# Kernel tuning notes

Measured on AMD Instinct MI355X. Metric: run time of the kernel, lower is better.

## Reference

```python
import jax, jax.numpy as jnp
import numpy as np

EPS = 1e-5


def _gcn_conv(x, src, dst, norm, W, b, n_nodes):
    # PyG GCNConv: transform, then normalized scatter-add aggregation (self-loops included in src/dst)
    h = x @ W                                   # [N, out]
    msg = h[src] * norm[:, None]                # gather over edges [E+N, out]
    agg = jax.ops.segment_sum(msg, dst, num_segments=n_nodes)
    return agg + b


def _bn(x, gamma, beta):
    # BatchNorm1d in training mode: batch stats over node axis, biased variance
    mu = jnp.mean(x, axis=0)
    var = jnp.mean((x - mu) ** 2, axis=0)
    return (x - mu) * jax.lax.rsqrt(var + EPS) * gamma + beta


def setup_inputs() -> dict:
    key = jax.random.key(0)
    ks = jax.random.split(key, 8)
    N, E, F_in, H, F_out = 50000, 800000, 32, 96, 2
    x = jax.random.normal(ks[0], (N, F_in), dtype=jnp.float32)
    edge_index = jax.random.randint(ks[1], (2, E), 0, N, dtype=jnp.int64)
    def lin(k, fi, fo):
        s = 1.0 / np.sqrt(fi)
        return jax.random.uniform(k, (fi, fo), jnp.float32, -s, s)
    W1 = lin(ks[2], F_in, H); b1 = jnp.zeros((H,), jnp.float32)
    W2 = lin(ks[3], H, H);    b2 = jnp.zeros((H,), jnp.float32)
    W3 = lin(ks[4], H, H);    b3 = jnp.zeros((H,), jnp.float32)
    W4 = lin(ks[5], H, F_out); b4 = jnp.zeros((F_out,), jnp.float32)
    g1 = jnp.ones((H,), jnp.float32); be1 = jnp.zeros((H,), jnp.float32)
    g2 = jnp.ones((H,), jnp.float32); be2 = jnp.zeros((H,), jnp.float32)
    g3 = jnp.ones((H,), jnp.float32); be3 = jnp.zeros((H,), jnp.float32)
    return dict(x=x, edge_index=edge_index,
                W1=W1, b1=b1, g1=g1, be1=be1,
                W2=W2, b2=b2, g2=g2, be2=be2,
                W3=W3, b3=b3, g3=g3, be3=be3,
                W4=W4, b4=b4)


def reference(x, edge_index, W1, b1, g1, be1, W2, b2, g2, be2, W3, b3, g3, be3, W4, b4):
    N = x.shape[0]
    loop = jnp.arange(N, dtype=edge_index.dtype)
    src = jnp.concatenate([edge_index[0], loop])   # add self-loops
    dst = jnp.concatenate([edge_index[1], loop])
    deg = jax.ops.segment_sum(jnp.ones_like(dst, dtype=x.dtype), dst, num_segments=N)
    dinv = jnp.where(deg > 0, jax.lax.rsqrt(deg), 0.0)
    norm = dinv[src] * dinv[dst]                   # D^{-1/2} (A+I) D^{-1/2}

    h = jax.nn.relu(_bn(_gcn_conv(x, src, dst, norm, W1, b1, N), g1, be1))
    h = jax.nn.relu(_bn(_gcn_conv(h, src, dst, norm, W2, b2, N), g2, be2))
    h = jax.nn.relu(_bn(_gcn_conv(h, src, dst, norm, W3, b3, N), g3, be3))
    return _gcn_conv(h, src, dst, norm, W4, b4, N)
```

## Files before the change

### kernel.cpp

```cpp
#include <hip/hip_runtime.h>
#include <hip/hip_bf16.h>

using bf16x8 = __attribute__((ext_vector_type(8))) short;
using f32x4  = __attribute__((ext_vector_type(4))) float;

__device__ __forceinline__ float ldf(const void* p, size_t i, float isf){
  if (isf > 0.5f) return ((const float*)p)[i];
  unsigned int u = ((unsigned int)((const unsigned short*)p)[i]) << 16;
  return __uint_as_float(u);
}
__device__ __forceinline__ unsigned short f2bf(float v){
  unsigned int u = __float_as_uint(v);
  u = (u + 0x7FFFu + ((u >> 16) & 1u)) >> 16;
  return (unsigned short)u;
}
__device__ __forceinline__ unsigned int pk2(float a, float b){
  return (unsigned int)f2bf(a) | ((unsigned int)f2bf(b) << 16);
}
__device__ __forceinline__ float lo16(unsigned int u){ return __uint_as_float(u << 16); }
__device__ __forceinline__ float hi16(unsigned int u){ return __uint_as_float(u & 0xFFFF0000u); }

__global__ void k_fill(unsigned short* o, unsigned short v, int n){
  int i = blockIdx.x*blockDim.x + threadIdx.x;
  if (i < n) o[i] = v;
}

__global__ void k_prep(const unsigned short* xh, const unsigned int* eu,
                       float* flag, int nelemX, long long E,
                       const void* W1, const void* W2, const void* W3, const void* W4,
                       unsigned short* __restrict__ Wt1, unsigned short* __restrict__ Wt2,
                       unsigned short* __restrict__ Wt3, float* __restrict__ W4f,
                       int* __restrict__ cnt, float* __restrict__ stAll, int n){
  int t = threadIdx.x;
  if (blockIdx.x > 0){
    int total = n + 4608;
    for (int i = (int)(blockIdx.x-1)*256 + t; i < total; i += (int)(gridDim.x-1)*256){
      if (i < n) cnt[i] = 0; else stAll[i - n] = 0.f;
    }
    return;
  }
  __shared__ int sf32, si64;
  __shared__ float sisf;
  if (t == 0){ sf32 = 0; si64 = 1; }
  __syncthreads();
  {
    int i = 2*t;
    if (i < nelemX){
      unsigned e8 = (xh[i] >> 7) & 0xFFu;
      if (e8 >= 140u) sf32 = 1;
    }
    if ((long long)(2*t + 1) < 2*E){
      if (eu[2*t + 1] != 0u) si64 = 0;
    }
  }
  __syncthreads();
  if (t == 0){
    flag[0] = (float)sf32; flag[1] = (float)si64;
    sisf = (float)sf32;
  }
  __syncthreads();
  float isf = sisf;
  for (int q = t; q < 3072; q += 256){
    int nn = q >> 5, k = q & 31;
    Wt1[q] = f2bf(ldf(W1, (size_t)96*k + nn, isf));
  }
  for (int q = t; q < 9216; q += 256){
    int nn = q/96, k = q - 96*nn;
    Wt2[q] = f2bf(ldf(W2, (size_t)96*k + nn, isf));
    Wt3[q] = f2bf(ldf(W3, (size_t)96*k + nn, isf));
  }
  if (t < 192) W4f[t] = ldf(W4, t, isf);
}

__global__ void k_cnt(const int* __restrict__ ei, const float* __restrict__ flag,
                      int* __restrict__ cnt, long long E, int n){
  long long i = (long long)blockIdx.x*blockDim.x + threadIdx.x;
  if (i >= E) return;
  int d = (flag[1] > 0.5f) ? ei[2*E + 2*i] : ei[E + i];
  if ((unsigned)d < (unsigned)n) atomicAdd(&cnt[d], 1);
}

__global__ void k_scan(const int* __restrict__ cnt, int* __restrict__ rowst,
                       int* __restrict__ cursor, float* __restrict__ dinv, int n){
  __shared__ int woff[16];
  __shared__ int chtot;
  __shared__ int carry_s;
  int tid = threadIdx.x;
  int lane = tid & 63, wid = tid >> 6;
  if (tid == 0) carry_s = 0;
  __syncthreads();
  for (int base = 0; base < n; base += 1024){
    int i = base + tid;
    int v = (i < n) ? cnt[i] : 0;
    int s = v;
    #pragma unroll
    for (int off = 1; off < 64; off <<= 1){
      int u = __shfl_up(s, off, 64);
      if (lane >= off) s += u;
    }
    if (lane == 63) woff[wid] = s;
    __syncthreads();
    if (tid < 16){
      int w = woff[tid];
      int ws_ = w;
      #pragma unroll
      for (int off = 1; off < 16; off <<= 1){
        int u = __shfl_up(ws_, off, 64);
        if (tid >= off) ws_ += u;
      }
      woff[tid] = ws_ - w;
      if (tid == 15) chtot = ws_;
    }
    __syncthreads();
    int carry = carry_s;
    if (i < n){
      int r = carry + woff[wid] + s - v;
      rowst[i] = r;
      cursor[i] = r;
      dinv[i]  = rsqrtf((float)(1 + v));
    }
    __syncthreads();
    if (tid == 0) carry_s = carry + chtot;
  }
  __syncthreads();
  if (tid == 0) rowst[n] = carry_s;
}

#define FS_CHUNK 4096
template<typename IT>
__global__ __launch_bounds__(256) void k_fl1(const int* __restrict__ ei,
      const float* __restrict__ flag, int* __restrict__ cursor, IT* __restrict__ csr,
      long long E, int n, int gF8,
      const void* __restrict__ x, const unsigned short* __restrict__ Wt1b,
      const float* __restrict__ dinv, unsigned short* __restrict__ HS){
  __shared__ __align__(16) unsigned short Xs[64][40];
  __shared__ __align__(16) unsigned short Wt[96][40];
  int t = threadIdx.x;
  if ((int)blockIdx.x < gF8){
    int part = blockIdx.x & 7;
    long long base = (long long)(blockIdx.x >> 3) * FS_CHUNK;
    int pl = (int)(((long long)n *  part     ) >> 3);
    int pr = (int)(((long long)n * (part + 1)) >> 3);
    bool i64 = (flag[1] > 0.5f);
    long long lim = base + FS_CHUNK < E ? base + FS_CHUNK : E;
    for (long long i = base + t; i < lim; i += 256){
      int s, d;
      if (i64){ s = ei[2*i]; d = ei[2*E + 2*i]; }
      else    { s = ei[i];   d = ei[E + i];     }
      if (d >= pl && d < pr && (unsigned)s < (unsigned)n){
        int p = atomicAdd(&cursor[d], 1);
        csr[p] = (IT)s;
      }
    }
    return;
  }
  int bid = blockIdx.x - gF8;
  float isf = flag[0];
  for (int q = t; q < 384; q += 256){
    uint4 v = ((const uint4*)Wt1b)[q];
    *(uint4*)&Wt[q >> 2][(q & 3)*8] = v;
  }
  {
    int row = t >> 2, part = t & 3;
    int node = bid*64 + row;
    uint4 o;
    if (node < n){
      if (isf > 0.5f){
        const float* xr = (const float*)x + (size_t)32*node + 8*part;
        o.x = pk2(xr[0], xr[1]); o.y = pk2(xr[2], xr[3]);
        o.z = pk2(xr[4], xr[5]); o.w = pk2(xr[6], xr[7]);
      } else {
        o = ((const uint4*)x)[(size_t)4*node + part];
      }
    } else { o.x = o.y = o.z = o.w = 0u; }
    *(uint4*)&Xs[row][8*part] = o;
  }
  __syncthreads();

  int wv = t >> 6, lane = t & 63;
  int m = lane & 15, quad = lane >> 4;
  bf16x8 av = *(const bf16x8*)&Xs[16*wv + m][8*quad];
  f32x4 acc[6];
  #pragma unroll
  for (int c = 0; c < 6; ++c) acc[c] = (f32x4)(0.f);
  #pragma unroll
  for (int c = 0; c < 6; ++c){
    bf16x8 bv = *(const bf16x8*)&Wt[16*c + m][8*quad];
    acc[c] = __builtin_amdgcn_mfma_f32_16x16x32_bf16(av, bv, acc[c], 0, 0, 0);
  }
  int rowbase = bid*64 + 16*wv + 4*quad;
  float div[4];
  #pragma unroll
  for (int r = 0; r < 4; ++r){ int rr = rowbase + r; div[r] = (rr < n) ? dinv[rr] : 0.f; }
  #pragma unroll
  for (int c = 0; c < 6; ++c){
    int col = 16*c + m;
    #pragma unroll
    for (int r = 0; r < 4; ++r){
      int rr = rowbase + r;
      if (rr < n) HS[(size_t)96*rr + col] = f2bf(acc[c][r]*div[r]);
    }
  }
}

#define ACC8(v) { a0+=lo16((v).x); a1+=hi16((v).x); a2+=lo16((v).y); a3+=hi16((v).y); \
                  a4+=lo16((v).z); a5+=hi16((v).z); a6+=lo16((v).w); a7+=hi16((v).w); }
template<typename IT>
__global__ __launch_bounds__(192) void k_agg(const uint4* __restrict__ hsr,
      const int* __restrict__ rowst, const IT* __restrict__ csr,
      const float* __restrict__ dinv, uint4* __restrict__ zb4,
      float* __restrict__ stout, int n){
  __shared__ float ls[16][97], lq[16][97];
  int g = threadIdx.x, ty = threadIdx.y;
  int t = ty*12 + g;
  int node = blockIdx.x*16 + ty;
  float r[8];
  if (node < n){
    uint4 v = hsr[(size_t)node*12 + g];
    float a0 = lo16(v.x), a1 = hi16(v.x), a2 = lo16(v.y), a3 = hi16(v.y);
    float a4 = lo16(v.z), a5 = hi16(v.z), a6 = lo16(v.w), a7 = hi16(v.w);
    int b = rowst[node], e = rowst[node+1];
    int j = b;
    for (; j + 7 < e; j += 8){
      uint4 v0 = hsr[(size_t)csr[j]  *12 + g];
      uint4 v1 = hsr[(size_t)csr[j+1]*12 + g];
      uint4 v2 = hsr[(size_t)csr[j+2]*12 + g];
      uint4 v3 = hsr[(size_t)csr[j+3]*12 + g];
      uint4 v4 = hsr[(size_t)csr[j+4]*12 + g];
      uint4 v5 = hsr[(size_t)csr[j+5]*12 + g];
      uint4 v6 = hsr[(size_t)csr[j+6]*12 + g];
      uint4 v7 = hsr[(size_t)csr[j+7]*12 + g];
      ACC8(v0); ACC8(v1); ACC8(v2); ACC8(v3);
      ACC8(v4); ACC8(v5); ACC8(v6); ACC8(v7);
    }
    for (; j + 3 < e; j += 4){
      uint4 v0 = hsr[(size_t)csr[j]  *12 + g];
      uint4 v1 = hsr[(size_t)csr[j+1]*12 + g];
      uint4 v2 = hsr[(size_t)csr[j+2]*12 + g];
      uint4 v3 = hsr[(size_t)csr[j+3]*12 + g];
      ACC8(v0); ACC8(v1); ACC8(v2); ACC8(v3);
    }
    for (; j < e; ++j){
      uint4 vv = hsr[(size_t)csr[j]*12 + g];
      ACC8(vv);
    }
    float di = dinv[node];
    uint4 o;
    o.x = pk2(a0*di, a1*di);
    o.y = pk2(a2*di, a3*di);
    o.z = pk2(a4*di, a5*di);
    o.w = pk2(a6*di, a7*di);
    zb4[(size_t)node*12 + g] = o;
    r[0]=lo16(o.x); r[1]=hi16(o.x); r[2]=lo16(o.y); r[3]=hi16(o.y);
    r[4]=lo16(o.z); r[5]=hi16(o.z); r[6]=lo16(o.w); r[7]=hi16(o.w);
  } else {
    #pragma unroll
    for (int jj = 0; jj < 8; ++jj) r[jj] = 0.f;
  }
  #pragma unroll
  for (int jj = 0; jj < 8; ++jj){
    ls[ty][8*g + jj] = r[jj];
    lq[ty][8*g + jj] = r[jj]*r[jj];
  }
  __syncthreads();
  if (t < 96){
    float s = 0.f, q = 0.f;
    #pragma unroll
    for (int rr = 0; rr < 16; ++rr){ s += ls[rr][t]; q += lq[rr][t]; }
    int rep = blockIdx.x & 7;
    atomicAdd(&stout[192*rep + t],      s);
    atomicAdd(&stout[192*rep + 96 + t], q);
  }
}

__global__ __launch_bounds__(256) void k_linm(const unsigned short* __restrict__ zb,
      const unsigned short* __restrict__ Wtb, const float* __restrict__ st,
      const void* __restrict__ gam, const void* __restrict__ bet,
      const float* __restrict__ flag, const float* __restrict__ dinv,
      unsigned short* __restrict__ HS, int n, float invN){
  __shared__ float sa[96], sc[96];
  __shared__ __align__(16) unsigned short Ys[64][104];
  __shared__ __align__(16) unsigned short Wt[96][104];
  int t = threadIdx.x;
  if (t < 96){
    float ssum = 0.f, qsum = 0.f;
    #pragma unroll
    for (int r = 0; r < 8; ++r){ ssum += st[192*r + t]; qsum += st[192*r + 96 + t]; }
    float isf = flag[0];
    float mu  = ssum*invN;
    float var = fmaxf(qsum*invN - mu*mu, 0.f);
    float istd = rsqrtf(var + 1e-5f);
    float a = ldf(gam, t, isf)*istd;
    sa[t] = a; sc[t] = ldf(bet, t, isf) - mu*a;
  }
  for (int q = t; q < 1152; q += 256){
    uint4 v = ((const uint4*)Wtb)[q];
    *(uint4*)&Wt[q/12][8*(q - 12*(q/12))] = v;
  }
  __syncthreads();
  {
    int row = t >> 2, part = t & 3;
    int node = blockIdx.x*64 + row;
    if (node < n){
      const uint4* zr = (const uint4*)(zb + (size_t)96*node) + 3*part;
      #pragma unroll
      for (int q = 0; q < 3; ++q){
        uint4 zz = zr[q];
        int k = 24*part + 8*q;
        float y0 = fmaxf(lo16(zz.x)*sa[k]   + sc[k],   0.f);
        float y1 = fmaxf(hi16(zz.x)*sa[k+1] + sc[k+1], 0.f);
        float y2 = fmaxf(lo16(zz.y)*sa[k+2] + sc[k+2], 0.f);
        float y3 = fmaxf(hi16(zz.y)*sa[k+3] + sc[k+3], 0.f);
        float y4 = fmaxf(lo16(zz.z)*sa[k+4] + sc[k+4], 0.f);
        float y5 = fmaxf(hi16(zz.z)*sa[k+5] + sc[k+5], 0.f);
        float y6 = fmaxf(lo16(zz.w)*sa[k+6] + sc[k+6], 0.f);
        float y7 = fmaxf(hi16(zz.w)*sa[k+7] + sc[k+7], 0.f);
        *(unsigned int*)&Ys[row][k]     = pk2(y0, y1);
        *(unsigned int*)&Ys[row][k + 2] = pk2(y2, y3);
        *(unsigned int*)&Ys[row][k + 4] = pk2(y4, y5);
        *(unsigned int*)&Ys[row][k + 6] = pk2(y6, y7);
      }
    } else {
      unsigned int* yp = (unsigned int*)&Ys[row][24*part];
      #pragma unroll
      for (int q = 0; q < 12; ++q) yp[q] = 0u;
    }
  }
  __syncthreads();

  int wv = t >> 6, lane = t & 63;
  int m = lane & 15, quad = lane >> 4;
  bf16x8 av[3];
  #pragma unroll
  for (int kt = 0; kt < 3; ++kt)
    av[kt] = *(const bf16x8*)&Ys[16*wv + m][32*kt + 8*quad];
  f32x4 acc[6];
  #pragma unroll
  for (int c = 0; c < 6; ++c) acc[c] = (f32x4)(0.f);
  #pragma unroll
  for (int c = 0; c < 6; ++c){
    const unsigned short* wrow = &Wt[16*c + m][8*quad];
    #pragma unroll
    for (int kt = 0; kt < 3; ++kt){
      bf16x8 bv = *(const bf16x8*)(wrow + 32*kt);
      acc[c] = __builtin_amdgcn_mfma_f32_16x16x32_bf16(av[kt], bv, acc[c], 0, 0, 0);
    }
  }
  int rowbase = blockIdx.x*64 + 16*wv + 4*quad;
  float div[4];
  #pragma unroll
  for (int r = 0; r < 4; ++r){ int rr = rowbase + r; div[r] = (rr < n) ? dinv[rr] : 0.f; }
  #pragma unroll
  for (int c = 0; c < 6; ++c){
    int col = 16*c + m;
    #pragma unroll
    for (int r = 0; r < 4; ++r){
      int rr = rowbase + r;
      if (rr < n) HS[(size_t)96*rr + col] = f2bf(acc[c][r]*div[r]);
    }
  }
}

__global__ __launch_bounds__(256) void k_lin4(const unsigned short* __restrict__ zb,
      const float* __restrict__ Wf, const float* __restrict__ st,
      const void* __restrict__ gam, const void* __restrict__ bet,
      const float* __restrict__ flag, const float* __restrict__ dinv,
      float* __restrict__ hs2, int n, float invN){
  __shared__ float sa[96], sc[96];
  int t = threadIdx.x;
  if (t < 96){
    float ssum = 0.f, qsum = 0.f;
    #pragma unroll
    for (int r = 0; r < 8; ++r){ ssum += st[192*r + t]; qsum += st[192*r + 96 + t]; }
    float isf = flag[0];
    float mu  = ssum*invN;
    float var = fmaxf(qsum*invN - mu*mu, 0.f);
    float istd = rsqrtf(var + 1e-5f);
    float a = ldf(gam, t, isf)*istd;
    sa[t] = a; sc[t] = ldf(bet, t, isf) - mu*a;
  }
  __syncthreads();
  int i = blockIdx.x*blockDim.x + t;
  if (i >= n) return;
  const uint4* zr = (const uint4*)(zb + (size_t)96*i);
  float a0 = 0.f, a1 = 0.f;
  #pragma unroll
  for (int q = 0; q < 12; ++q){
    uint4 zz = zr[q];
    int k = 8*q;
    float y;
    y = fmaxf(lo16(zz.x)*sa[k]   + sc[k],   0.f); a0 += y*Wf[2*k];    a1 += y*Wf[2*k+1];
    y = fmaxf(hi16(zz.x)*sa[k+1] + sc[k+1], 0.f); a0 += y*Wf[2*k+2];  a1 += y*Wf[2*k+3];
    y = fmaxf(lo16(zz.y)*sa[k+2] + sc[k+2], 0.f); a0 += y*Wf[2*k+4];  a1 += y*Wf[2*k+5];
    y = fmaxf(hi16(zz.y)*sa[k+3] + sc[k+3], 0.f); a0 += y*Wf[2*k+6];  a1 += y*Wf[2*k+7];
    y = fmaxf(lo16(zz.z)*sa[k+4] + sc[k+4], 0.f); a0 += y*Wf[2*k+8];  a1 += y*Wf[2*k+9];
    y = fmaxf(hi16(zz.z)*sa[k+5] + sc[k+5], 0.f); a0 += y*Wf[2*k+10]; a1 += y*Wf[2*k+11];
    y = fmaxf(lo16(zz.w)*sa[k+6] + sc[k+6], 0.f); a0 += y*Wf[2*k+12]; a1 += y*Wf[2*k+13];
    y = fmaxf(hi16(zz.w)*sa[k+7] + sc[k+7], 0.f); a0 += y*Wf[2*k+14]; a1 += y*Wf[2*k+15];
  }
  float di = dinv[i];
  hs2[(size_t)2*i]   = di*a0;
  hs2[(size_t)2*i+1] = di*a1;
}

template<typename IT>
__global__ void k_agg2(const float2* __restrict__ hs2, const int* __restrict__ rowst,
                       const IT* __restrict__ csr, const float* __restrict__ dinv,
                       const void* __restrict__ b4, const float* __restrict__ flag,
                       void* __restrict__ out, int n){
  int node = blockIdx.x*blockDim.x + threadIdx.x;
  if (node >= n) return;
  float2 a = hs2[node];
  int b = rowst[node], e = rowst[node+1];
  for (int j = b; j < e; ++j){
    float2 v = hs2[(size_t)csr[j]];
    a.x += v.x; a.y += v.y;
  }
  float isf = flag[0];
  float di = dinv[node];
  float v0 = a.x*di + ldf(b4, 0, isf);
  float v1 = a.y*di + ldf(b4, 1, isf);
  if (isf > 0.5f){
    ((float*)out)[(size_t)2*node]   = v0;
    ((float*)out)[(size_t)2*node+1] = v1;
  } else {
    ((unsigned short*)out)[(size_t)2*node]   = f2bf(v0);
    ((unsigned short*)out)[(size_t)2*node+1] = f2bf(v1);
  }
}

extern "C" void kernel_launch(void* const* d_in, const int* in_sizes, int n_in,
                              void* d_out, int out_size, void* d_ws, size_t ws_size,
                              hipStream_t stream)
{
  const int B = 256;
  unsigned short* outh = (unsigned short*)d_out;

  if (n_in < 16){
    k_fill<<<(out_size+B-1)/B, B, 0, stream>>>(outh, 0x3F40u, out_size); return;
  }
  const int N = in_sizes[0] / 32;
  const long long E = in_sizes[1] / 2;
  if (in_sizes[0] % 32 != 0 || out_size != 2*N){
    k_fill<<<(out_size+B-1)/B, B, 0, stream>>>(outh, 0x3F60u, out_size); return;
  }
  const bool u16 = (N < 65536);

  size_t Npad = ((size_t)N + 3) & ~(size_t)3;
  float* ws   = (float*)d_ws;
  float* dinv = ws;
  float* hs2  = dinv + Npad;
  float* flag = hs2 + (size_t)2*N;
  float* stAll= flag + 4;
  float* W4f  = stAll + 4608;
  unsigned short* Wt1b = (unsigned short*)(W4f + 192);
  unsigned short* Wt2b = Wt1b + 3072;
  unsigned short* Wt3b = Wt2b + 9216;
  int* cnt    = (int*)(Wt3b + 9216);
  int* cursor = cnt + N;
  int* rowst  = cursor + N;
  void* csrv  = (void*)(rowst + N + 1);
  size_t csrBytes = (size_t)E * (u16 ? 2 : 4);
  uintptr_t hp_ = (uintptr_t)csrv + csrBytes;
  hp_ = (hp_ + 15) & ~(uintptr_t)15;
  unsigned short* HS = (unsigned short*)hp_;
  unsigned short* Zb = HS + (size_t)96*N;

  size_t needB = ((uintptr_t)(Zb + (size_t)96*N) - (uintptr_t)d_ws) + 64;
  if (ws_size < needB){
    k_fill<<<(out_size+B-1)/B, B, 0, stream>>>(outh, 0x3F00u, out_size); return;
  }

  const void* x  = d_in[0];
  const int*  ei = (const int*)d_in[1];
  const void* W1 = d_in[2];
  const void* g1 = d_in[4];  const void* be1 = d_in[5];
  const void* W2 = d_in[6];
  const void* g2 = d_in[8];  const void* be2 = d_in[9];
  const void* W3 = d_in[10];
  const void* g3 = d_in[12]; const void* be3 = d_in[13];
  const void* W4 = d_in[14];
  const void* b4 = d_in[15];

  float* stA = stAll;
  float* stB = stAll + 1536;
  float* stC = stAll + 3072;

  int gN  = (N + B - 1)/B;
  int gE  = (int)((E + B - 1)/B);
  int gA  = (N + 15)/16;
  int gL  = (N + 63)/64;
  int gF8 = (int)((E + FS_CHUNK - 1)/FS_CHUNK) * 8;
  float invN = 1.0f / (float)N;
  dim3 ablk(12,16);

  k_prep<<<33, B, 0, stream>>>((const unsigned short*)x, (const unsigned int*)ei,
                               flag, in_sizes[0], E, W1, W2, W3, W4,
                               Wt1b, Wt2b, Wt3b, W4f, cnt, stAll, N);
  k_cnt<<<gE, B, 0, stream>>>(ei, flag, cnt, E, N);
  k_scan<<<1, 1024, 0, stream>>>(cnt, rowst, cursor, dinv, N);

  if (u16){
    unsigned short* csr = (unsigned short*)csrv;
    k_fl1<unsigned short><<<gF8 + gL, B, 0, stream>>>(ei, flag, cursor, csr, E, N, gF8,
                                                      x, Wt1b, dinv, HS);
    k_agg<unsigned short><<<gA, ablk, 0, stream>>>((const uint4*)HS, rowst, csr, dinv, (uint4*)Zb, stA, N);
    k_linm<<<gL, B, 0, stream>>>(Zb, Wt2b, stA, g1, be1, flag, dinv, HS, N, invN);
    k_agg<unsigned short><<<gA, ablk, 0, stream>>>((const uint4*)HS, rowst, csr, dinv, (uint4*)Zb, stB, N);
    k_linm<<<gL, B, 0, stream>>>(Zb, Wt3b, stB, g2, be2, flag, dinv, HS, N, invN);
    k_agg<unsigned short><<<gA, ablk, 0, stream>>>((const uint4*)HS, rowst, csr, dinv, (uint4*)Zb, stC, N);
    k_lin4<<<gN, B, 0, stream>>>(Zb, W4f, stC, g3, be3, flag, dinv, hs2, N, invN);
    k_agg2<unsigned short><<<gN, B, 0, stream>>>((const float2*)hs2, rowst, csr, dinv, b4, flag, d_out, N);
  } else {
    int* csr = (int*)csrv;
    k_fl1<int><<<gF8 + gL, B, 0, stream>>>(ei, flag, cursor, csr, E, N, gF8,
                                           x, Wt1b, dinv, HS);
    k_agg<int><<<gA, ablk, 0, stream>>>((const uint4*)HS, rowst, csr, dinv, (uint4*)Zb, stA, N);
    k_linm<<<gL, B, 0, stream>>>(Zb, Wt2b, stA, g1, be1, flag, dinv, HS, N, invN);
    k_agg<int><<<gA, ablk, 0, stream>>>((const uint4*)HS, rowst, csr, dinv, (uint4*)Zb, stB, N);
    k_linm<<<gL, B, 0, stream>>>(Zb, Wt3b, stB, g2, be2, flag, dinv, HS, N, invN);
    k_agg<int><<<gA, ablk, 0, stream>>>((const uint4*)HS, rowst, csr, dinv, (uint4*)Zb, stC, N);
    k_lin4<<<gN, B, 0, stream>>>(Zb, W4f, stC, g3, be3, flag, dinv, hs2, N, invN);
    k_agg2<int><<<gN, B, 0, stream>>>((const float2*)hs2, rowst, csr, dinv, b4, flag, d_out, N);
  }
}
```

Baseline: 381.7 us.

## Replace single-block prefix scan with multi-block atomic segment allocation

```diff
diff --git a/kernel.cpp b/kernel.cpp
--- a/kernel.cpp
+++ b/kernel.cpp
@@ -33,7 +33,7 @@
                        int* __restrict__ cnt, float* __restrict__ stAll, int n){
   int t = threadIdx.x;
   if (blockIdx.x > 0){
-    int total = n + 4608;
+    int total = n + 4609;
     for (int i = (int)(blockIdx.x-1)*256 + t; i < total; i += (int)(gridDim.x-1)*256){
       if (i < n) cnt[i] = 0; else stAll[i - n] = 0.f;
     }
@@ -80,50 +80,28 @@
   if ((unsigned)d < (unsigned)n) atomicAdd(&cnt[d], 1);
 }
 
-__global__ void k_scan(const int* __restrict__ cnt, int* __restrict__ rowst,
-                       int* __restrict__ cursor, float* __restrict__ dinv, int n){
-  __shared__ int woff[16];
-  __shared__ int chtot;
-  __shared__ int carry_s;
-  int tid = threadIdx.x;
-  int lane = tid & 63, wid = tid >> 6;
-  if (tid == 0) carry_s = 0;
-  __syncthreads();
-  for (int base = 0; base < n; base += 1024){
-    int i = base + tid;
-    int v = (i < n) ? cnt[i] : 0;
-    int s = v;
-    #pragma unroll
-    for (int off = 1; off < 64; off <<= 1){
-      int u = __shfl_up(s, off, 64);
-      if (lane >= off) s += u;
-    }
-    if (lane == 63) woff[wid] = s;
-    __syncthreads();
-    if (tid < 16){
-      int w = woff[tid];
-      int ws_ = w;
-      #pragma unroll
-      for (int off = 1; off < 16; off <<= 1){
-        int u = __shfl_up(ws_, off, 64);
-        if (tid >= off) ws_ += u;
-      }
-      woff[tid] = ws_ - w;
-      if (tid == 15) chtot = ws_;
-    }
-    __syncthreads();
-    int carry = carry_s;
-    if (i < n){
-      int r = carry + woff[wid] + s - v;
-      rowst[i] = r;
-      cursor[i] = r;
-      dinv[i]  = rsqrtf((float)(1 + v));
-    }
-    __syncthreads();
-    if (tid == 0) carry_s = carry + chtot;
-  }
-  __syncthreads();
-  if (tid == 0) rowst[n] = carry_s;
+__global__ void k_emit2(const int* __restrict__ cnt, int* __restrict__ gctr,
+                        int* __restrict__ rowst, int* __restrict__ cursor,
+                        float* __restrict__ dinv, int n){
+  int i = blockIdx.x*256 + threadIdx.x;
+  int lane = threadIdx.x & 63;
+  int v = (i < n) ? cnt[i] : 0;
+  int s = v;
+  #pragma unroll
+  for (int off = 1; off < 64; off <<= 1){
+    int u = __shfl_up(s, off, 64);
+    if (lane >= off) s += u;
+  }
+  int wtot = __shfl(s, 63, 64);
+  int base = 0;
+  if (lane == 63) base = atomicAdd(gctr, wtot);
+  base = __shfl(base, 63, 64);
+  if (i < n){
+    int r = base + s - v;
+    rowst[i]  = r;
+    cursor[i] = r;
+    dinv[i]   = rsqrtf((float)(1 + v));
+  }
 }
 
 #define FS_CHUNK 4096
@@ -207,7 +185,8 @@
                   a4+=lo16((v).z); a5+=hi16((v).z); a6+=lo16((v).w); a7+=hi16((v).w); }
 template<typename IT>
 __global__ __launch_bounds__(192) void k_agg(const uint4* __restrict__ hsr,
-      const int* __restrict__ rowst, const IT* __restrict__ csr,
+      const int* __restrict__ rowst, const int* __restrict__ cnt,
+      const IT* __restrict__ csr,
       const float* __restrict__ dinv, uint4* __restrict__ zb4,
       float* __restrict__ stout, int n){
   __shared__ float ls[16][97], lq[16][97];
@@ -219,7 +198,7 @@
     uint4 v = hsr[(size_t)node*12 + g];
     float a0 = lo16(v.x), a1 = hi16(v.x), a2 = lo16(v.y), a3 = hi16(v.y);
     float a4 = lo16(v.z), a5 = hi16(v.z), a6 = lo16(v.w), a7 = hi16(v.w);
-    int b = rowst[node], e = rowst[node+1];
+    int b = rowst[node], e = b + cnt[node];
     int j = b;
     for (; j + 7 < e; j += 8){
       uint4 v0 = hsr[(size_t)csr[j]  *12 + g];
@@ -405,13 +384,14 @@
 
 template<typename IT>
 __global__ void k_agg2(const float2* __restrict__ hs2, const int* __restrict__ rowst,
-                       const IT* __restrict__ csr, const float* __restrict__ dinv,
+                       const int* __restrict__ cnt, const IT* __restrict__ csr,
+                       const float* __restrict__ dinv,
                        const void* __restrict__ b4, const float* __restrict__ flag,
                        void* __restrict__ out, int n){
   int node = blockIdx.x*blockDim.x + threadIdx.x;
   if (node >= n) return;
   float2 a = hs2[node];
-  int b = rowst[node], e = rowst[node+1];
+  int b = rowst[node], e = b + cnt[node];
   for (int j = b; j < e; ++j){
     float2 v = hs2[(size_t)csr[j]];
     a.x += v.x; a.y += v.y;
@@ -452,14 +432,14 @@
   float* hs2  = dinv + Npad;
   float* flag = hs2 + (size_t)2*N;
   float* stAll= flag + 4;
-  float* W4f  = stAll + 4608;
+  float* W4f  = stAll + 4612;
   unsigned short* Wt1b = (unsigned short*)(W4f + 192);
   unsigned short* Wt2b = Wt1b + 3072;
   unsigned short* Wt3b = Wt2b + 9216;
   int* cnt    = (int*)(Wt3b + 9216);
   int* cursor = cnt + N;
   int* rowst  = cursor + N;
-  void* csrv  = (void*)(rowst + N + 1);
+  void* csrv  = (void*)(rowst + N);
   size_t csrBytes = (size_t)E * (u16 ? 2 : 4);
   uintptr_t hp_ = (uintptr_t)csrv + csrBytes;
   hp_ = (hp_ + 15) & ~(uintptr_t)15;
@@ -485,9 +465,11 @@
   float* stA = stAll;
   float* stB = stAll + 1536;
   float* stC = stAll + 3072;
+  int*   gctr = (int*)(stAll + 4608);
 
   int gN  = (N + B - 1)/B;
   int gE  = (int)((E + B - 1)/B);
+  int nb  = (N + 255)/256;
   int gA  = (N + 15)/16;
   int gL  = (N + 63)/64;
   int gF8 = (int)((E + FS_CHUNK - 1)/FS_CHUNK) * 8;
@@ -498,29 +480,29 @@
                                flag, in_sizes[0], E, W1, W2, W3, W4,
                                Wt1b, Wt2b, Wt3b, W4f, cnt, stAll, N);
   k_cnt<<<gE, B, 0, stream>>>(ei, flag, cnt, E, N);
-  k_scan<<<1, 1024, 0, stream>>>(cnt, rowst, cursor, dinv, N);
+  k_emit2<<<nb, B, 0, stream>>>(cnt, gctr, rowst, cursor, dinv, N);
 
   if (u16){
     unsigned short* csr = (unsigned short*)csrv;
     k_fl1<unsigned short><<<gF8 + gL, B, 0, stream>>>(ei, flag, cursor, csr, E, N, gF8,
                                                       x, Wt1b, dinv, HS);
-    k_agg<unsigned short><<<gA, ablk, 0, stream>>>((const uint4*)HS, rowst, csr, dinv, (uint4*)Zb, stA, N);
+    k_agg<unsigned short><<<gA, ablk, 0, stream>>>((const uint4*)HS, rowst, cnt, csr, dinv, (uint4*)Zb, stA, N);
     k_linm<<<gL, B, 0, stream>>>(Zb, Wt2b, stA, g1, be1, flag, dinv, HS, N, invN);
-    k_agg<unsigned short><<<gA, ablk, 0, stream>>>((const uint4*)HS, rowst, csr, dinv, (uint4*)Zb, stB, N);
+    k_agg<unsigned short><<<gA, ablk, 0, stream>>>((const uint4*)HS, rowst, cnt, csr, dinv, (uint4*)Zb, stB, N);
     k_linm<<<gL, B, 0, stream>>>(Zb, Wt3b, stB, g2, be2, flag, dinv, HS, N, invN);
-    k_agg<unsigned short><<<gA, ablk, 0, stream>>>((const uint4*)HS, rowst, csr, dinv, (uint4*)Zb, stC, N);
+    k_agg<unsigned short><<<gA, ablk, 0, stream>>>((const uint4*)HS, rowst, cnt, csr, dinv, (uint4*)Zb, stC, N);
     k_lin4<<<gN, B, 0, stream>>>(Zb, W4f, stC, g3, be3, flag, dinv, hs2, N, invN);
-    k_agg2<unsigned short><<<gN, B, 0, stream>>>((const float2*)hs2, rowst, csr, dinv, b4, flag, d_out, N);
+    k_agg2<unsigned short><<<gN, B, 0, stream>>>((const float2*)hs2, rowst, cnt, csr, dinv, b4, flag, d_out, N);
   } else {
     int* csr = (int*)csrv;
     k_fl1<int><<<gF8 + gL, B, 0, stream>>>(ei, flag, cursor, csr, E, N, gF8,
                                            x, Wt1b, dinv, HS);
-    k_agg<int><<<gA, ablk, 0, stream>>>((const uint4*)HS, rowst, csr, dinv, (uint4*)Zb, stA, N);
+    k_agg<int><<<gA, ablk, 0, stream>>>((const uint4*)HS, rowst, cnt, csr, dinv, (uint4*)Zb, stA, N);
     k_linm<<<gL, B, 0, stream>>>(Zb, Wt2b, stA, g1, be1, flag, dinv, HS, N, invN);
-    k_agg<int><<<gA, ablk, 0, stream>>>((const uint4*)HS, rowst, csr, dinv, (uint4*)Zb, stB, N);
+    k_agg<int><<<gA, ablk, 0, stream>>>((const uint4*)HS, rowst, cnt, csr, dinv, (uint4*)Zb, stB, N);
     k_linm<<<gL, B, 0, stream>>>(Zb, Wt3b, stB, g2, be2, flag, dinv, HS, N, invN);
-    k_agg<int><<<gA, ablk, 0, stream>>>((const uint4*)HS, rowst, csr, dinv, (uint4*)Zb, stC, N);
+    k_agg<int><<<gA, ablk, 0, stream>>>((const uint4*)HS, rowst, cnt, csr, dinv, (uint4*)Zb, stC, N);
     k_lin4<<<gN, B, 0, stream>>>(Zb, W4f, stC, g3, be3, flag, dinv, hs2, N, invN);
-    k_agg2<int><<<gN, B, 0, stream>>>((const float2*)hs2, rowst, csr, dinv, b4, flag, d_out, N);
-  }
-}
+    k_agg2<int><<<gN, B, 0, stream>>>((const float2*)hs2, rowst, cnt, csr, dinv, b4, flag, d_out, N);
+  }
+}
```

Measured after the change: 340.8 us. 10.7% less time.
